# Performance work log

Measured on AMD Instinct MI355X. Metric: run time of the kernel, lower is better.

## Reference

```python
import jax, jax.numpy as jnp
import numpy as np

# (u, v) frequency bands, taken mod 8 as in the torch module
FREQ_BANDS = np.array([[0, 1], [1, 0], [1, 1], [2, 2], [3, 3], [4, 4]]) % 8


def setup_inputs() -> dict:
    key = jax.random.key(0)
    x = jax.random.normal(key, (64, 3, 512, 512), dtype=jnp.float32)
    return {"x": x}


def reference(x):
    B, C, H, W = x.shape
    gh, gw = H // 8, W // 8
    # unfold(2,8,8).unfold(3,8,8) -> [B, C, gh, gw, 8, 8]
    patches = x.reshape(B, C, gh, 8, gw, 8).transpose(0, 1, 2, 4, 3, 5)
    # 2D FFT over each 8x8 block, magnitude
    dct = jnp.abs(jnp.fft.fft2(patches))  # [B, C, gh, gw, 8, 8]
    # freq_mask only keeps the bins we index below, so masking is a no-op
    # for the gathered bins; gather all bands at once (vectorized over bands)
    u = jnp.asarray(FREQ_BANDS[:, 0])
    v = jnp.asarray(FREQ_BANDS[:, 1])
    band = dct[..., u, v]                 # [B, C, gh, gw, n_bands]
    feats = band.mean(axis=(2, 3))        # [B, C, n_bands]
    return feats.reshape(B, -1)           # [B, C * n_bands]
```

## Files before the change

### kernel.cpp

```cpp
#include <hip/hip_runtime.h>
#include <math.h>


#define IMG_H 512
#define IMG_W 512

__global__ __launch_bounds__(256) void dct_band_kernel(const float* __restrict__ x,
                                                       float* __restrict__ out) {
    const int wg   = blockIdx.x;
    const int img  = wg >> 4;
    const int rg   = wg & 15;
    const int t    = threadIdx.x;
    const int brow = rg * 4 + (t >> 6);
    const int bcol = t & 63;

    const float* p = x + (size_t)img * (IMG_H * IMG_W)
                       + (size_t)(brow * 8) * IMG_W + bcol * 8;

    const float C1 = 0.70710678118654752440f;
    const float ct[8] = {1.f,  C1, 0.f, -C1, -1.f, -C1, 0.f,  C1};
    const float st[8] = {0.f,  C1, 1.f,  C1,  0.f, -C1, -1.f, -C1};

    float F01r = 0.f, F01i = 0.f;
    float F10r = 0.f, F10i = 0.f;
    float F11r = 0.f, F11i = 0.f;
    float F22r = 0.f, F22i = 0.f;
    float F33r = 0.f, F33i = 0.f;
    float F44  = 0.f;

#pragma unroll
    for (int i = 0; i < 8; ++i) {
        const float4 a = *(const float4*)(p + (size_t)i * IMG_W);
        const float4 b = *(const float4*)(p + (size_t)i * IMG_W + 4);
        const float x0 = a.x, x1 = a.y, x2 = a.z, x3 = a.w;
        const float x4 = b.x, x5 = b.y, x6 = b.z, x7 = b.w;

        const float g0  = x0 + x1 + x2 + x3 + x4 + x5 + x6 + x7;
        const float g1r = x0 - x4 + C1 * (x1 - x3 - x5 + x7);
        const float g1i = -(C1 * (x1 + x3 - x5 - x7) + x2 - x6);
        const float g2r = x0 - x2 + x4 - x6;
        const float g2i = -(x1 - x3 + x5 - x7);
        const float g3r = x0 - x4 + C1 * (-x1 + x3 + x5 - x7);
        const float g3i = -(C1 * (x1 + x3 - x5 - x7) - x2 + x6);
        const float g4  = x0 - x1 + x2 - x3 + x4 - x5 + x6 - x7;

        const float c1 = ct[i],           s1 = st[i];
        const float c2 = ct[(2 * i) & 7], s2 = st[(2 * i) & 7];
        const float c3 = ct[(3 * i) & 7], s3 = st[(3 * i) & 7];

        F01r += g1r;             F01i += g1i;
        F10r += g0 * c1;         F10i -= g0 * s1;
        F11r += g1r * c1 + g1i * s1;   F11i += g1i * c1 - g1r * s1;
        F22r += g2r * c2 + g2i * s2;   F22i += g2i * c2 - g2r * s2;
        F33r += g3r * c3 + g3i * s3;   F33i += g3i * c3 - g3r * s3;
        F44  += (i & 1) ? -g4 : g4;
    }

    float m[6];
    m[0] = sqrtf(F01r * F01r + F01i * F01i);
    m[1] = sqrtf(F10r * F10r + F10i * F10i);
    m[2] = sqrtf(F11r * F11r + F11i * F11i);
    m[3] = sqrtf(F22r * F22r + F22i * F22i);
    m[4] = sqrtf(F33r * F33r + F33i * F33i);
    m[5] = fabsf(F44);

#pragma unroll
    for (int off = 32; off > 0; off >>= 1) {
#pragma unroll
        for (int k = 0; k < 6; ++k) m[k] += __shfl_down(m[k], off);
    }

    __shared__ float red[4][6];
    const int wave = t >> 6;
    if ((t & 63) == 0) {
#pragma unroll
        for (int k = 0; k < 6; ++k) red[wave][k] = m[k];
    }
    __syncthreads();

    if (t < 6) {
        const float s = red[0][t] + red[1][t] + red[2][t] + red[3][t];
        atomicAdd(&out[img * 6 + t], s * (1.0f / 4096.0f));
    }
}

extern "C" void kernel_launch(void* const* d_in, const int* in_sizes, int n_in,
                              void* d_out, int out_size, void* d_ws, size_t ws_size,
                              hipStream_t stream) {
    const float* x = (const float*)d_in[0];
    float* out = (float*)d_out;

    hipMemsetAsync(d_out, 0, (size_t)out_size * sizeof(float), stream);

    const int n_imgs = 64 * 3;
    dim3 grid(n_imgs * 16);
    dim3 block(256);
    dct_band_kernel<<<grid, block, 0, stream>>>(x, out);
}
```

Measured before the change: 269.5 us.

## Remap lanes to half-blocks for coalesced float4 loads with shuffle combine

Each lane now owns a 4-column half of an 8x8 block, so a wave reads 1 KB of contiguous memory per row with fully coalesced float4 loads. All eight row loads are issued up front. The partial DFT over the four columns is merged with the neighbouring lane through an xor shuffle, using a sign twiddle for the odd half, and the normalisation becomes 1/8192 because both lanes of each pair hold the block's magnitudes. The grid doubles and each thread does half the work, at the cost of extra shuffles and duplicated magnitude math.

```diff
diff --git a/kernel.cpp b/kernel.cpp
--- a/kernel.cpp
+++ b/kernel.cpp
@@ -2,20 +2,26 @@
 #include <math.h>
 
 
-#define IMG_H 512
 #define IMG_W 512
+#define IMG_PIX (512 * 512)
 
 __global__ __launch_bounds__(256) void dct_band_kernel(const float* __restrict__ x,
                                                        float* __restrict__ out) {
-    const int wg   = blockIdx.x;
-    const int img  = wg >> 4;
-    const int rg   = wg & 15;
     const int t    = threadIdx.x;
-    const int brow = rg * 4 + (t >> 6);
-    const int bcol = t & 63;
+    const int lane = t & 63;
+    const int wave = t >> 6;
+    const int w    = blockIdx.x * 4 + wave;
+    const int img  = w >> 7;
+    const int bR   = (w >> 1) & 63;
+    const int half = w & 1;
 
-    const float* p = x + (size_t)img * (IMG_H * IMG_W)
-                       + (size_t)(brow * 8) * IMG_W + bcol * 8;
+    const float* p = x + (size_t)img * IMG_PIX
+                       + (size_t)(bR * 8) * IMG_W + half * 256 + lane * 4;
+
+    float4 row[8];
+#pragma unroll
+    for (int r = 0; r < 8; ++r)
+        row[r] = *(const float4*)(p + (size_t)r * IMG_W);
 
     const float C1 = 0.70710678118654752440f;
     const float ct[8] = {1.f,  C1, 0.f, -C1, -1.f, -C1, 0.f,  C1};
@@ -29,32 +35,49 @@
     float F44  = 0.f;
 
 #pragma unroll
-    for (int i = 0; i < 8; ++i) {
-        const float4 a = *(const float4*)(p + (size_t)i * IMG_W);
-        const float4 b = *(const float4*)(p + (size_t)i * IMG_W + 4);
-        const float x0 = a.x, x1 = a.y, x2 = a.z, x3 = a.w;
-        const float x4 = b.x, x5 = b.y, x6 = b.z, x7 = b.w;
+    for (int k = 0; k < 4; ++k) {
+        const float x0 = (&row[0].x)[k];
+        const float x1 = (&row[1].x)[k];
+        const float x2 = (&row[2].x)[k];
+        const float x3 = (&row[3].x)[k];
+        const float x4 = (&row[4].x)[k];
+        const float x5 = (&row[5].x)[k];
+        const float x6 = (&row[6].x)[k];
+        const float x7 = (&row[7].x)[k];
 
-        const float g0  = x0 + x1 + x2 + x3 + x4 + x5 + x6 + x7;
-        const float g1r = x0 - x4 + C1 * (x1 - x3 - x5 + x7);
-        const float g1i = -(C1 * (x1 + x3 - x5 - x7) + x2 - x6);
-        const float g2r = x0 - x2 + x4 - x6;
-        const float g2i = -(x1 - x3 + x5 - x7);
-        const float g3r = x0 - x4 + C1 * (-x1 + x3 + x5 - x7);
-        const float g3i = -(C1 * (x1 + x3 - x5 - x7) - x2 + x6);
-        const float g4  = x0 - x1 + x2 - x3 + x4 - x5 + x6 - x7;
+        const float h0  = x0 + x1 + x2 + x3 + x4 + x5 + x6 + x7;
+        const float h1r = x0 - x4 + C1 * (x1 - x3 - x5 + x7);
+        const float h1i = -(C1 * (x1 + x3 - x5 - x7) + x2 - x6);
+        const float h2r = x0 - x2 + x4 - x6;
+        const float h2i = -(x1 - x3 + x5 - x7);
+        const float h3r = x0 - x4 + C1 * (-x1 + x3 + x5 - x7);
+        const float h3i = -(C1 * (x1 + x3 - x5 - x7) - x2 + x6);
+        const float h4  = x0 - x1 + x2 - x3 + x4 - x5 + x6 - x7;
 
-        const float c1 = ct[i],           s1 = st[i];
-        const float c2 = ct[(2 * i) & 7], s2 = st[(2 * i) & 7];
-        const float c3 = ct[(3 * i) & 7], s3 = st[(3 * i) & 7];
+        const float c1 = ct[k],           s1 = st[k];
+        const float c2 = ct[(2 * k) & 7], s2 = st[(2 * k) & 7];
+        const float c3 = ct[(3 * k) & 7], s3 = st[(3 * k) & 7];
+        const float w4 = (k & 1) ? -1.f : 1.f;
 
-        F01r += g1r;             F01i += g1i;
-        F10r += g0 * c1;         F10i -= g0 * s1;
-        F11r += g1r * c1 + g1i * s1;   F11i += g1i * c1 - g1r * s1;
-        F22r += g2r * c2 + g2i * s2;   F22i += g2i * c2 - g2r * s2;
-        F33r += g3r * c3 + g3i * s3;   F33i += g3i * c3 - g3r * s3;
-        F44  += (i & 1) ? -g4 : g4;
+        F01r += h0 * c1;               F01i -= h0 * s1;
+        F10r += h1r;                   F10i += h1i;
+        F11r += h1r * c1 + h1i * s1;   F11i += h1i * c1 - h1r * s1;
+        F22r += h2r * c2 + h2i * s2;   F22i += h2i * c2 - h2r * s2;
+        F33r += h3r * c3 + h3i * s3;   F33i += h3i * c3 - h3r * s3;
+        F44  += h4 * w4;
     }
+
+    const float sgn = (lane & 1) ? -1.f : 1.f;
+    F01r *= sgn; F01i *= sgn;
+    F11r *= sgn; F11i *= sgn;
+    F33r *= sgn; F33i *= sgn;
+
+    F01r += __shfl_xor(F01r, 1); F01i += __shfl_xor(F01i, 1);
+    F10r += __shfl_xor(F10r, 1); F10i += __shfl_xor(F10i, 1);
+    F11r += __shfl_xor(F11r, 1); F11i += __shfl_xor(F11i, 1);
+    F22r += __shfl_xor(F22r, 1); F22i += __shfl_xor(F22i, 1);
+    F33r += __shfl_xor(F33r, 1); F33i += __shfl_xor(F33i, 1);
+    F44  += __shfl_xor(F44, 1);
 
     float m[6];
     m[0] = sqrtf(F01r * F01r + F01i * F01i);
@@ -71,8 +94,7 @@
     }
 
     __shared__ float red[4][6];
-    const int wave = t >> 6;
-    if ((t & 63) == 0) {
+    if (lane == 0) {
 #pragma unroll
         for (int k = 0; k < 6; ++k) red[wave][k] = m[k];
     }
@@ -80,7 +102,7 @@
 
     if (t < 6) {
         const float s = red[0][t] + red[1][t] + red[2][t] + red[3][t];
-        atomicAdd(&out[img * 6 + t], s * (1.0f / 4096.0f));
+        atomicAdd(&out[img * 6 + t], s * (1.0f / 8192.0f));
     }
 }
 
@@ -92,8 +114,7 @@
 
     hipMemsetAsync(d_out, 0, (size_t)out_size * sizeof(float), stream);
 
-    const int n_imgs = 64 * 3;
-    dim3 grid(n_imgs * 16);
+    dim3 grid(6144);
     dim3 block(256);
     dct_band_kernel<<<grid, block, 0, stream>>>(x, out);
 }
```

Result: no change. 270.5 us (+0.4%).
